# Optimization experiments

Hardware: AMD Instinct MI355X
Metric: run time of the kernel (lower is better)

The kernel has to match this reference:

```python
import jax, jax.numpy as jnp
import numpy as np

H, L, N = 512, 4096, 64

def make_dplr_hippo(n):
    # HiPPO-LegS -> NPLR -> DPLR diagonalization (numpy, init-time only)
    p0 = np.sqrt(1 + 2 * np.arange(n))
    A = p0[:, None] * p0[None, :]
    A = -(np.tril(A) - np.diag(np.arange(n)))
    p = np.sqrt(np.arange(n) + 0.5)
    b = np.sqrt(2 * np.arange(n) + 1.0)
    S = A + p[:, None] * p[None, :]
    Lambda_re = np.full(n, np.diagonal(S).mean())
    Lambda_im, V = np.linalg.eigh(S * -1j)
    Pc = V.conj().T @ p
    Bc = V.conj().T @ b
    return Lambda_re, Lambda_im, Pc, Bc

def setup_inputs() -> dict:
    key = jax.random.key(0)
    k_u, k_c, k_s = jax.random.split(key, 3)
    lr, li, Pc, Bc = make_dplr_hippo(N)
    tile = lambda v: jnp.tile(jnp.asarray(v, jnp.float32)[None, :], (H, 1))
    dt_min, dt_max = 0.001, 0.1
    log_step = (jax.random.uniform(k_s, (H, 1), jnp.float32)
                * (np.log(dt_max) - np.log(dt_min)) + np.log(dt_min))
    return {
        "u": jax.random.normal(k_u, (H, L), jnp.float32),
        "Lambda_re": tile(lr), "Lambda_im": tile(li),
        "P_re": tile(Pc.real), "P_im": tile(Pc.imag),
        "B_re": tile(Bc.real), "B_im": tile(Bc.imag),
        "C": jax.random.normal(k_c, (H, N, 2), jnp.float32) * (0.5 ** 0.5),
        "D": jnp.ones((H, 1), jnp.float32),
        "log_step": log_step,
    }

def reference(u, Lambda_re, Lambda_im, P_re, P_im, B_re, B_im, C, D, log_step):
    # u: [H, L]; all params leading dim H (vmapped channels)
    Lam = jnp.minimum(Lambda_re, -1e-4) + 1j * Lambda_im      # [H, N]
    P = P_re + 1j * P_im                                       # [H, N]
    B = B_re + 1j * B_im                                       # [H, N]
    Cc = C[..., 0] + 1j * C[..., 1]                             # [H, N]
    step = jnp.exp(log_step)                                    # [H, 1]
    Lseq = u.shape[-1]
    Omega = jnp.exp(-2j * jnp.pi * (jnp.arange(Lseq) / Lseq)).astype(jnp.complex64)  # [L]
    g = (2.0 / step) * ((1.0 - Omega) / (1.0 + Omega))[None, :]  # [H, L]
    c = 2.0 / (1.0 + Omega)                                      # [L]
    denom = 1.0 / (g[:, :, None] - Lam[:, None, :])              # [H, L, N]
    cauchy = lambda v: jnp.einsum('hn,hln->hl', v, denom)
    k00 = cauchy(Cc.conj() * B)
    k01 = cauchy(Cc.conj() * P)
    k10 = cauchy(P.conj() * B)
    k11 = cauchy(P.conj() * P)
    atRoots = c[None, :] * (k00 - k01 * (1.0 / (1.0 + k11)) * k10)
    K = jnp.fft.ifft(atRoots, Lseq, axis=-1).real                # [H, L] conv kernel
    # causal convolution via zero-padded FFT (length 2L)
    ud = jnp.fft.rfft(u, n=2 * Lseq, axis=-1)
    Kd = jnp.fft.rfft(K, n=2 * Lseq, axis=-1)
    y = jnp.fft.irfft(ud * Kd, n=2 * Lseq, axis=-1)[..., :Lseq]
    return y + D * u
```

## Files before the change

kernel.cpp:

```cpp
#include <hip/hip_runtime.h>
#include <math.h>

#define NT 512

typedef float v2 __attribute__((ext_vector_type(2)));

__device__ __forceinline__ v2 vrot(v2 a){ return (v2){-a.y, a.x}; }
__device__ __forceinline__ v2 vconj(v2 a){ return (v2){a.x, -a.y}; }
__device__ __forceinline__ v2 vcmul(v2 a, v2 b){ return a.x*b + a.y*vrot(b); }
__device__ __forceinline__ v2 vfma1(float s, v2 v, v2 acc){
    return (v2){ __builtin_fmaf(s, v.x, acc.x), __builtin_fmaf(s, v.y, acc.y) };
}

__device__ __forceinline__ int SW(int e){ return e ^ (((e>>5) ^ (e>>9)) & 15); }

__device__ __forceinline__ int d8r4(int x){
    return ((x&7)<<9) | (((x>>3)&7)<<6) | (((x>>6)&7)<<3) | ((x>>9)&7);
}
__device__ __forceinline__ int rev3(int t){
    return ((t&7)<<6) | (t&56) | ((t>>6)&7);
}

__device__ __forceinline__ void dft8_inv(v2 t[8], v2 y[8]) {
    const float RH = 0.70710678f;
    v2 p  = t[0]+t[4], m  = t[0]-t[4], q  = t[2]+t[6], r  = t[2]-t[6];
    v2 rr = vrot(r);
    v2 E0 = p+q, E2 = p-q, E1 = m+rr, E3 = m-rr;
    v2 p2 = t[1]+t[5], m2 = t[1]-t[5], q2 = t[3]+t[7], r2 = t[3]-t[7];
    v2 rr2 = vrot(r2);
    v2 O0 = p2+q2, O2 = p2-q2, O1 = m2+rr2, O3 = m2-rr2;
    v2 W1O = RH*(O1 + vrot(O1));
    v2 W2O = vrot(O2);
    v2 W3O = vrot(RH*(O3 + vrot(O3)));
    y[0] = E0 + O0;  y[4] = E0 - O0;
    y[1] = E1 + W1O; y[5] = E1 - W1O;
    y[2] = E2 + W2O; y[6] = E2 - W2O;
    y[3] = E3 + W3O; y[7] = E3 - W3O;
}

__device__ __forceinline__ void dft8_fwd(v2 t[8], v2 y[8]) {
    const float RH = 0.70710678f;
    v2 p  = t[0]+t[4], m  = t[0]-t[4], q  = t[2]+t[6], r  = t[2]-t[6];
    v2 rr = vrot(r);
    v2 E0 = p+q, E2 = p-q, E1 = m-rr, E3 = m+rr;
    v2 p2 = t[1]+t[5], m2 = t[1]-t[5], q2 = t[3]+t[7], r2 = t[3]-t[7];
    v2 rr2 = vrot(r2);
    v2 O0 = p2+q2, O2 = p2-q2, O1 = m2-rr2, O3 = m2+rr2;
    v2 W1O = RH*(O1 - vrot(O1));
    v2 W2O = (v2){O2.y, -O2.x};
    v2 W3O = (-RH)*(O3 + vrot(O3));
    y[0] = E0 + O0;  y[4] = E0 - O0;
    y[1] = E1 + W1O; y[5] = E1 - W1O;
    y[2] = E2 + W2O; y[6] = E2 - W2O;
    y[3] = E3 + W3O; y[7] = E3 - W3O;
}

__device__ __forceinline__ void apply_tw_inv(v2 t[8], float fm, int j) {
    float sb, cb; __sincosf(fm*(float)j, &sb, &cb);
    v2 W1 = (v2){cb, sb};
    v2 W2 = vcmul(W1,W1), W3 = vcmul(W1,W2), W4 = vcmul(W2,W2),
       W5 = vcmul(W2,W3), W6 = vcmul(W3,W3), W7 = vcmul(W3,W4);
    t[1]=vcmul(t[1],W1); t[2]=vcmul(t[2],W2); t[3]=vcmul(t[3],W3);
    t[4]=vcmul(t[4],W4); t[5]=vcmul(t[5],W5); t[6]=vcmul(t[6],W6);
    t[7]=vcmul(t[7],W7);
}

template<int Q>
__device__ __forceinline__ void r8_dit_inv(v2* buf, int tid) {
    int j = tid & (Q-1);
    int base = 8*tid - 7*j;
    v2 t[8];
    #pragma unroll
    for (int k = 0; k < 8; ++k) t[k] = buf[SW(base + k*Q)];
    apply_tw_inv(t, 6.2831853072f / (float)(8*Q), j);
    v2 y[8];
    dft8_inv(t, y);
    #pragma unroll
    for (int m = 0; m < 8; ++m) buf[SW(base + m*Q)] = y[m];
    __syncthreads();
}

template<int Q>
__device__ __forceinline__ void r8_dif_fwd(v2* buf, int tid) {
    int j = tid & (Q-1);
    int baseL = 8*tid - 7*j;
    v2 W1=(v2){1.0f,0.0f},W2=W1,W3=W1,W4=W1,W5=W1,W6=W1,W7=W1;
    if (Q > 1) {
        const float fm = -6.2831853072f / (float)(8*Q);
        float sb, cb; __sincosf(fm*(float)j, &sb, &cb);
        W1 = (v2){cb, sb};
        W2 = vcmul(W1,W1); W3 = vcmul(W1,W2); W4 = vcmul(W2,W2);
        W5 = vcmul(W2,W3); W6 = vcmul(W3,W3); W7 = vcmul(W3,W4);
    }
    #pragma unroll 1
    for (int hh = 0; hh < 2; ++hh) {
        int base = baseL + (hh << 12);
        v2 t[8];
        #pragma unroll
        for (int k = 0; k < 8; ++k) t[k] = buf[SW(base + k*Q)];
        v2 y[8];
        dft8_fwd(t, y);
        if (Q > 1) {
            y[1]=vcmul(y[1],W1); y[2]=vcmul(y[2],W2); y[3]=vcmul(y[3],W3);
            y[4]=vcmul(y[4],W4); y[5]=vcmul(y[5],W5); y[6]=vcmul(y[6],W6);
            y[7]=vcmul(y[7],W7);
        }
        #pragma unroll
        for (int m = 0; m < 8; ++m) buf[SW(base + m*Q)] = y[m];
    }
    __syncthreads();
}

__global__ void __launch_bounds__(NT)
s4_fused(const float* __restrict__ u,
         const float* __restrict__ Lre, const float* __restrict__ Lim,
         const float* __restrict__ Pre, const float* __restrict__ Pim,
         const float* __restrict__ Bre, const float* __restrict__ Bim,
         const float* __restrict__ Cin, const float* __restrict__ Din,
         const float* __restrict__ logstep,
         float* __restrict__ out)
{
    __shared__ v2 buf[8192];
    const int tid = threadIdx.x;
    const int h = blockIdx.x;

    v2* par = buf + 4096;
    if (tid < 64) {
        const int n = tid;
        float lre = fminf(Lre[h*64+n], -1e-4f);
        float lim = Lim[h*64+n];
        par[n] = (v2){lre, lim};
        float pr = Pre[h*64+n], pi = Pim[h*64+n];
        float br = Bre[h*64+n], bi = Bim[h*64+n];
        float cr = Cin[h*128+2*n], ci = Cin[h*128+2*n+1];
        v2 cc = (v2){cr, -ci};
        par[64+n]  = vcmul(cc, (v2){br, bi});
        par[128+n] = vcmul(cc, (v2){pr, pi});
        v2 pc = (v2){pr, -pi};
        par[192+n] = vcmul(pc, (v2){br, bi});
        par[256+n] = (v2){pr*pr + pi*pi, 0.0f};
    }
    __syncthreads();

    const float step = expf(logstep[h]);
    const float tos  = 2.0f / step;

    v2 a4[4];
    #pragma unroll 1
    for (int hp = 0; hp < 2; ++hp) {
        v2 g[4], cf[4], k00[4], k01[4], k10[4], k11[4];
        const int lbase = hp*(4*NT);
        #pragma unroll
        for (int i = 0; i < 4; ++i) {
            int l = lbase + i*NT + tid;
            float ang = -6.2831855f * ((float)l * (1.0f/4096.0f));
            double ds, dc;
            sincos((double)ang, &ds, &dc);
            float Omx = (float)dc, Omy = (float)ds;
            float nx = 1.0f-Omx, ny = -Omy;
            float dx = 1.0f+Omx, dy =  Omy;
            float dinv = 1.0f/(dx*dx + dy*dy);
            g[i]  = (v2){tos*((nx*dx+ny*dy)*dinv), tos*((ny*dx-nx*dy)*dinv)};
            cf[i] = (v2){2.0f*dx*dinv, -2.0f*dy*dinv};
            k00[i]=(v2)(0.0f); k01[i]=(v2)(0.0f); k10[i]=(v2)(0.0f); k11[i]=(v2)(0.0f);
        }
        #pragma unroll 1
        for (int n = 0; n < 64; ++n) {
            v2 lam = par[n];
            v2 w00 = par[64+n], w01 = par[128+n], w10 = par[192+n];
            float w11r = par[256+n].x;
            #pragma unroll
            for (int i = 0; i < 4; ++i) {
                v2 d = g[i] - lam;
                float inv = __builtin_amdgcn_rcpf(d.x*d.x + d.y*d.y);
                v2 p  = d * inv;
                v2 cp = (v2){p.x, -p.y};
                v2 rp = (v2){p.y,  p.x};
                k00[i] = vfma1(w00.y, rp, vfma1(w00.x, cp, k00[i]));
                k01[i] = vfma1(w01.y, rp, vfma1(w01.x, cp, k01[i]));
                k10[i] = vfma1(w10.y, rp, vfma1(w10.x, cp, k10[i]));
                k11[i] = vfma1(w11r,  cp, k11[i]);
            }
        }
        #pragma unroll
        for (int i = 0; i < 4; ++i) {
            v2 opk = (v2){1.0f + k11[i].x, k11[i].y};
            float iv = 1.0f/(opk.x*opk.x + opk.y*opk.y);
            v2 r11 = vconj(opk) * iv;
            v2 t  = vcmul(vcmul(k01[i], r11), k10[i]);
            v2 res = vcmul(cf[i], k00[i] - t);
            if (hp == 0) buf[SW(tid + 512*i)] = res;
            else         a4[i] = res;
        }
    }
    {
        v2 t[8];
        #pragma unroll
        for (int k = 0; k < 4; ++k) t[k] = buf[SW(tid + 512*k)];
        #pragma unroll
        for (int k = 0; k < 4; ++k) t[4+k] = a4[k];
        __syncthreads();
        v2 y[8];
        dft8_inv(t, y);
        int tb8 = 8*rev3(tid);
        #pragma unroll
        for (int m = 0; m < 8; ++m) buf[SW(tb8 + m)] = y[m];
    }
    __syncthreads();

    r8_dit_inv<8 >(buf, tid);
    r8_dit_inv<64>(buf, tid);

    {
        v2 t[8];
        #pragma unroll
        for (int k = 0; k < 8; ++k) t[k] = buf[SW(tid + 512*k)];
        apply_tw_inv(t, 6.2831853072f / 4096.0f, tid);
        v2 y[8];
        dft8_inv(t, y);
        float uval[8];
        const float* up = u + h*4096;
        #pragma unroll
        for (int m = 0; m < 8; ++m) uval[m] = up[tid + 512*m];
        __syncthreads();
        float s2, c2; __sincosf(-6.2831853072f/8192.0f*(float)tid, &s2, &c2);
        v2 cur = (v2){c2, s2};
        const v2 C16n = (v2){0.92387953f, -0.38268343f};
        #pragma unroll
        for (int m = 0; m < 8; ++m) {
            int l = tid + 512*m;
            v2 z = (v2){uval[m], y[m].x * (1.0f/4096.0f)};
            buf[SW(l)]      = z;
            buf[SW(l+4096)] = vcmul(z, cur);
            cur = vcmul(cur, C16n);
        }
    }
    __syncthreads();

    r8_dif_fwd<512>(buf, tid);
    r8_dif_fwd<64 >(buf, tid);
    r8_dif_fwd<8  >(buf, tid);
    r8_dif_fwd<1  >(buf, tid);

    {
        float sb, cb; __sincosf(6.2831853072f/8192.0f*(float)tid, &sb, &cb);
        v2 cur = (v2){cb, sb};
        const v2 C16p = (v2){0.92387953f, 0.38268343f};
        v2 v[8];
        #pragma unroll 1
        for (int i = 0; i < 8; ++i) {
            int r  = i*NT + tid;
            int k1 = r,        k1c = (8192 - r) & 8191;
            int k2 = r + 4096, k2c = 4096 - r;
            v2 za = buf[SW(((k1 &1)<<12) + d8r4(k1 >>1))];
            v2 zb = buf[SW(((k1c&1)<<12) + d8r4(k1c>>1))];
            v2 zc = buf[SW(((k2 &1)<<12) + d8r4(k2 >>1))];
            v2 zd = buf[SW(((k2c&1)<<12) + d8r4(k2c>>1))];
            v2 U1 = 0.5f*(za + vconj(zb));
            v2 K1 = -0.5f*vrot(za - vconj(zb));
            v2 Yr = vcmul(U1, K1);
            v2 U2 = 0.5f*(zc + vconj(zd));
            v2 K2 = -0.5f*vrot(zc - vconj(zd));
            v2 Ys = vcmul(U2, K2);
            v[i] = (Yr + Ys) + vrot(vcmul(cur, Yr - Ys));
            cur = vcmul(cur, C16p);
        }
        __syncthreads();
        v2 y[8];
        dft8_inv(v, y);
        int tb8 = 8*rev3(tid);
        #pragma unroll
        for (int m = 0; m < 8; ++m) buf[SW(tb8 + m)] = y[m];
    }
    __syncthreads();

    r8_dit_inv<8 >(buf, tid);
    r8_dit_inv<64>(buf, tid);

    {
        v2 t[8];
        #pragma unroll
        for (int k = 0; k < 8; ++k) t[k] = buf[SW(tid + 512*k)];
        apply_tw_inv(t, 6.2831853072f / 4096.0f, tid);
        v2 y[8];
        dft8_inv(t, y);
        const float Dh = Din[h];
        const float sc = 1.0f / 8192.0f;
        const v2* u2 = (const v2*)(u + h*4096);
        v2*     out2 = (v2*)(out + h*4096);
        #pragma unroll
        for (int m = 0; m < 4; ++m) {
            int n = tid + 512*m;
            out2[n] = sc*y[m] + Dh*u2[n];
        }
    }
}

extern "C" void kernel_launch(void* const* d_in, const int* in_sizes, int n_in,
                              void* d_out, int out_size, void* d_ws, size_t ws_size,
                              hipStream_t stream)
{
    const float* u       = (const float*)d_in[0];
    const float* Lre     = (const float*)d_in[1];
    const float* Lim     = (const float*)d_in[2];
    const float* Pre     = (const float*)d_in[3];
    const float* Pim     = (const float*)d_in[4];
    const float* Bre     = (const float*)d_in[5];
    const float* Bim     = (const float*)d_in[6];
    const float* Cin     = (const float*)d_in[7];
    const float* Din     = (const float*)d_in[8];
    const float* logstep = (const float*)d_in[9];
    float* out = (float*)d_out;
    const int H = in_sizes[8];
    hipLaunchKernelGGL(s4_fused, dim3(H), dim3(NT), 0, stream,
                       u, Lre, Lim, Pre, Pim, Bre, Bim, Cin, Din, logstep, out);
}
```

Before: 171.9 us.

## Use purely imaginary bilinear frequencies and move parameter prep to a separate kernel

```diff
diff --git a/kernel.cpp b/kernel.cpp
--- a/kernel.cpp
+++ b/kernel.cpp
@@ -111,69 +111,77 @@
     __syncthreads();
 }
 
+__global__ void __launch_bounds__(64)
+s4_prep(const float* __restrict__ Lre, const float* __restrict__ Lim,
+        const float* __restrict__ Pre, const float* __restrict__ Pim,
+        const float* __restrict__ Bre, const float* __restrict__ Bim,
+        const float* __restrict__ Cin,
+        float* __restrict__ ws8, float* __restrict__ ws1)
+{
+    int idx = blockIdx.x*64 + threadIdx.x;
+    float lre = fminf(Lre[idx], -1e-4f);
+    float lim = Lim[idx];
+    float pr = Pre[idx], pi = Pim[idx];
+    float br = Bre[idx], bi = Bim[idx];
+    float cr = Cin[2*idx], ci = Cin[2*idx+1];
+    v2 cc = (v2){cr, -ci};
+    v2 w00 = vcmul(cc, (v2){br, bi});
+    v2 w01 = vcmul(cc, (v2){pr, pi});
+    v2 w10 = vcmul((v2){pr,-pi}, (v2){br, bi});
+    float* o = ws8 + idx*8;
+    o[0] = -lre;  o[1] = -lim;
+    o[2] = w00.x; o[3] = w00.y;
+    o[4] = w01.x; o[5] = w01.y;
+    o[6] = w10.x; o[7] = w10.y;
+    ws1[idx] = pr*pr + pi*pi;
+}
+
 __global__ void __launch_bounds__(NT)
 s4_fused(const float* __restrict__ u,
-         const float* __restrict__ Lre, const float* __restrict__ Lim,
-         const float* __restrict__ Pre, const float* __restrict__ Pim,
-         const float* __restrict__ Bre, const float* __restrict__ Bim,
-         const float* __restrict__ Cin, const float* __restrict__ Din,
-         const float* __restrict__ logstep,
+         const float* __restrict__ Din, const float* __restrict__ logstep,
+         const float* __restrict__ ws8, const float* __restrict__ ws1,
          float* __restrict__ out)
 {
     __shared__ v2 buf[8192];
     const int tid = threadIdx.x;
     const int h = blockIdx.x;
 
-    v2* par = buf + 4096;
-    if (tid < 64) {
-        const int n = tid;
-        float lre = fminf(Lre[h*64+n], -1e-4f);
-        float lim = Lim[h*64+n];
-        par[n] = (v2){lre, lim};
-        float pr = Pre[h*64+n], pi = Pim[h*64+n];
-        float br = Bre[h*64+n], bi = Bim[h*64+n];
-        float cr = Cin[h*128+2*n], ci = Cin[h*128+2*n+1];
-        v2 cc = (v2){cr, -ci};
-        par[64+n]  = vcmul(cc, (v2){br, bi});
-        par[128+n] = vcmul(cc, (v2){pr, pi});
-        v2 pc = (v2){pr, -pi};
-        par[192+n] = vcmul(pc, (v2){br, bi});
-        par[256+n] = (v2){pr*pr + pi*pi, 0.0f};
-    }
-    __syncthreads();
-
     const float step = expf(logstep[h]);
     const float tos  = 2.0f / step;
+    const float hstep = 0.5f * step;
+    const float* pp = ws8 + (h*64)*8;
+    const float* pw = ws1 + h*64;
 
     v2 a4[4];
     #pragma unroll 1
     for (int hp = 0; hp < 2; ++hp) {
-        v2 g[4], cf[4], k00[4], k01[4], k10[4], k11[4];
+        float tv[4];
+        v2 cf[4], k00[4], k01[4], k10[4], k11[4];
         const int lbase = hp*(4*NT);
         #pragma unroll
         for (int i = 0; i < 4; ++i) {
             int l = lbase + i*NT + tid;
             float ang = -6.2831855f * ((float)l * (1.0f/4096.0f));
-            double ds, dc;
-            sincos((double)ang, &ds, &dc);
-            float Omx = (float)dc, Omy = (float)ds;
-            float nx = 1.0f-Omx, ny = -Omy;
-            float dx = 1.0f+Omx, dy =  Omy;
-            float dinv = 1.0f/(dx*dx + dy*dy);
-            g[i]  = (v2){tos*((nx*dx+ny*dy)*dinv), tos*((ny*dx-nx*dy)*dinv)};
-            cf[i] = (v2){2.0f*dx*dinv, -2.0f*dy*dinv};
+            float sh, ch; __sincosf(0.5f*ang, &sh, &ch);
+            float traw = -tos * sh * __builtin_amdgcn_rcpf(ch);
+            float t = fminf(fmaxf(traw, -1e18f), 1e18f);
+            tv[i] = t;
+            cf[i] = (v2){1.0f, t*hstep};
             k00[i]=(v2)(0.0f); k01[i]=(v2)(0.0f); k10[i]=(v2)(0.0f); k11[i]=(v2)(0.0f);
         }
         #pragma unroll 1
         for (int n = 0; n < 64; ++n) {
-            v2 lam = par[n];
-            v2 w00 = par[64+n], w01 = par[128+n], w10 = par[192+n];
-            float w11r = par[256+n].x;
+            float nlre = pp[n*8+0], nlim = pp[n*8+1];
+            v2 w00 = (v2){pp[n*8+2], pp[n*8+3]};
+            v2 w01 = (v2){pp[n*8+4], pp[n*8+5]};
+            v2 w10 = (v2){pp[n*8+6], pp[n*8+7]};
+            float w11r = pw[n];
+            float lre2 = nlre*nlre;
             #pragma unroll
             for (int i = 0; i < 4; ++i) {
-                v2 d = g[i] - lam;
-                float inv = __builtin_amdgcn_rcpf(d.x*d.x + d.y*d.y);
-                v2 p  = d * inv;
+                float s = tv[i] + nlim;
+                float inv = __builtin_amdgcn_rcpf(__builtin_fmaf(s, s, lre2));
+                v2 p = (v2){nlre, s} * inv;
                 v2 cp = (v2){p.x, -p.y};
                 v2 rp = (v2){p.y,  p.x};
                 k00[i] = vfma1(w00.y, rp, vfma1(w00.x, cp, k00[i]));
@@ -185,7 +193,7 @@
         #pragma unroll
         for (int i = 0; i < 4; ++i) {
             v2 opk = (v2){1.0f + k11[i].x, k11[i].y};
-            float iv = 1.0f/(opk.x*opk.x + opk.y*opk.y);
+            float iv = __builtin_amdgcn_rcpf(opk.x*opk.x + opk.y*opk.y);
             v2 r11 = vconj(opk) * iv;
             v2 t  = vcmul(vcmul(k01[i], r11), k10[i]);
             v2 res = vcmul(cf[i], k00[i] - t);
@@ -312,6 +320,12 @@
     const float* logstep = (const float*)d_in[9];
     float* out = (float*)d_out;
     const int H = in_sizes[8];
+
+    float* ws8 = (float*)d_ws;
+    float* ws1 = ws8 + (size_t)H*64*8;
+
+    hipLaunchKernelGGL(s4_prep, dim3(H), dim3(64), 0, stream,
+                       Lre, Lim, Pre, Pim, Bre, Bim, Cin, ws8, ws1);
     hipLaunchKernelGGL(s4_fused, dim3(H), dim3(NT), 0, stream,
-                       u, Lre, Lim, Pre, Pim, Bre, Bim, Cin, Din, logstep, out);
-}
+                       u, Din, logstep, ws8, ws1, out);
+}
```

Result: no change. 171.9 us (+0.0%).
